# Kernel tuning notes

Hardware: AMD Instinct MI355X
Metric: run time of the kernel (lower is better)

## Reference

```python
import jax, jax.numpy as jnp
import numpy as np

B, S, D, H, HD, I, L = 1, 2048, 1024, 16, 64, 2816, 2
EPS = 1e-5
ROPE_BASE = 10000.0


def rmsnorm(x, w):
    return x * jax.lax.rsqrt(jnp.mean(x * x, axis=-1, keepdims=True) + EPS) * w


def precompute_freqs_cis():
    # matches precompute_freqs_cis: [S, HD//2, 2] = (cos, sin)
    freqs = 1.0 / (ROPE_BASE ** (jnp.arange(0, HD, 2, dtype=jnp.float32) / HD))
    ang = jnp.outer(jnp.arange(S, dtype=jnp.float32), freqs)
    return jnp.stack([jnp.cos(ang), jnp.sin(ang)], axis=-1)


def apply_rope(x, fc):
    # x: [B,S,H,HD]; fc: [S,HD//2,2] -> interleaved pair rotation
    xs = x.reshape(*x.shape[:-1], HD // 2, 2)
    f = fc[None, :, None]  # [1,S,1,HD//2,2]
    out = jnp.stack([
        xs[..., 0] * f[..., 0] - xs[..., 1] * f[..., 1],
        xs[..., 1] * f[..., 0] + xs[..., 0] * f[..., 1],
    ], axis=-1)
    return out.reshape(x.shape)


def setup_inputs() -> dict:
    key = jax.random.key(0)
    ks = jax.random.split(key, 6)
    p = lambda k, shape: jax.random.normal(k, shape, jnp.float32) * 0.02
    return {
        "x": jax.random.normal(ks[0], (B, S, D), jnp.float32),
        "wqkv": p(ks[1], (L, 3 * H * HD, D)),
        "wo": p(ks[2], (L, D, H * HD)),
        "w1": p(ks[3], (L, I, D)),
        "w2": p(ks[4], (L, D, I)),
        "w3": p(ks[5], (L, I, D)),
        "attn_norm_w": jnp.ones((L, D), jnp.float32),
        "ffn_norm_w": jnp.ones((L, D), jnp.float32),
        "attn_ls": 0.01 * jnp.ones((L, D), jnp.float32),
        "ffn_ls": 0.01 * jnp.ones((L, D), jnp.float32),
        "final_norm_w": jnp.ones((D,), jnp.float32),
    }


def reference(x, wqkv, wo, w1, w2, w3, attn_norm_w, ffn_norm_w, attn_ls, ffn_ls, final_norm_w):
    fc = precompute_freqs_cis()
    causal = jnp.tril(jnp.ones((S, S), dtype=bool))  # [S,S]
    scale = 1.0 / np.sqrt(HD).astype(np.float32)
    h = x
    for l in range(L):
        # --- attention block ---
        xn = rmsnorm(h, attn_norm_w[l])
        qkv = xn @ wqkv[l].T  # [B,S,3*H*HD]
        q, k, v = jnp.split(qkv, 3, axis=-1)
        q = apply_rope(q.reshape(B, S, H, HD), fc)
        k = apply_rope(k.reshape(B, S, H, HD), fc)
        v = v.reshape(B, S, H, HD)
        scores = jnp.einsum('bqhd,bkhd->bhqk', q, k) * scale
        scores = jnp.where(causal, scores, jnp.finfo(scores.dtype).min)
        attn = jax.nn.softmax(scores, axis=-1)
        y = jnp.einsum('bhqk,bkhd->bqhd', attn, v).reshape(B, S, H * HD)
        h = h + (y @ wo[l].T) * attn_ls[l]
        # --- feed-forward block (SwiGLU) ---
        xn = rmsnorm(h, ffn_norm_w[l])
        ff = (jax.nn.silu(xn @ w1[l].T) * (xn @ w3[l].T)) @ w2[l].T
        h = h + ff * ffn_ls[l]
    return rmsnorm(h, final_norm_w)
```

## Files before the change

kernel.cpp:

```cpp
#include <hip/hip_runtime.h>
#include <math.h>

#define SEQ 2048
#define DIM 1024
#define NH 16
#define HDIM 64
#define IDIM 2816
#define NL 2

typedef __attribute__((ext_vector_type(8))) short bf16x8;
typedef __attribute__((ext_vector_type(4))) float f32x4;

__device__ __forceinline__ unsigned short f2bf(float f) {
    unsigned int u = __float_as_uint(f);
    u = (u + 0x7fffu + ((u >> 16) & 1u)) >> 16;
    return (unsigned short)u;
}
__device__ __forceinline__ float bf2f(unsigned short u) {
    return __uint_as_float((unsigned int)u << 16);
}

__device__ __forceinline__ void gl_lds16(const void* g, void* l) {
    __builtin_amdgcn_global_load_lds(
        (const __attribute__((address_space(1))) unsigned int*)g,
        (__attribute__((address_space(3))) unsigned int*)l, 16, 0, 0);
}

template <bool BF16OUT>
__global__ __launch_bounds__(256) void rmsnorm_kernel(const float* __restrict__ in,
                                                      const float* __restrict__ w,
                                                      void* __restrict__ out) {
    const int row = blockIdx.x;
    const int t = threadIdx.x;
    const float4 v = ((const float4*)(in + (size_t)row * DIM))[t];
    float ss = v.x * v.x + v.y * v.y + v.z * v.z + v.w * v.w;
#pragma unroll
    for (int m = 1; m < 64; m <<= 1) ss += __shfl_xor(ss, m);
    __shared__ float red[4];
    if ((t & 63) == 0) red[t >> 6] = ss;
    __syncthreads();
    const float tot = red[0] + red[1] + red[2] + red[3];
    const float r = 1.0f / sqrtf(tot * (1.0f / DIM) + 1e-5f);
    const float4 wv = ((const float4*)w)[t];
    float o0 = v.x * r * wv.x, o1 = v.y * r * wv.y;
    float o2 = v.z * r * wv.z, o3 = v.w * r * wv.w;
    if (BF16OUT) {
        ushort4 o = {f2bf(o0), f2bf(o1), f2bf(o2), f2bf(o3)};
        ((ushort4*)((unsigned short*)out + (size_t)row * DIM))[t] = o;
    } else {
        float4 o = {o0, o1, o2, o3};
        ((float4*)((float*)out + (size_t)row * DIM))[t] = o;
    }
}

#define WQKV_OFF 0
#define WO_OFF   3145728
#define W1_OFF   4194304
#define W3_OFF   7077888
#define W2_OFF   9961472
#define WTOT     12845056

__global__ __launch_bounds__(256) void convert_weights_kernel(
    const float* __restrict__ wqkv, const float* __restrict__ wo,
    const float* __restrict__ w1, const float* __restrict__ w3,
    const float* __restrict__ w2, unsigned short* __restrict__ out) {
    const size_t i8 = ((size_t)blockIdx.x * 256 + threadIdx.x) * 8;
    const float* src;
    size_t local;
    if (i8 < WO_OFF)      { src = wqkv; local = i8 - WQKV_OFF; }
    else if (i8 < W1_OFF) { src = wo;   local = i8 - WO_OFF; }
    else if (i8 < W3_OFF) { src = w1;   local = i8 - W1_OFF; }
    else if (i8 < W2_OFF) { src = w3;   local = i8 - W3_OFF; }
    else                  { src = w2;   local = i8 - W2_OFF; }
    const float4 v0 = *(const float4*)(src + local);
    const float4 v1 = *(const float4*)(src + local + 4);
    ushort4 o0 = {f2bf(v0.x), f2bf(v0.y), f2bf(v0.z), f2bf(v0.w)};
    ushort4 o1 = {f2bf(v1.x), f2bf(v1.y), f2bf(v1.z), f2bf(v1.w)};
    *(ushort4*)(out + i8) = o0;
    *(ushort4*)(out + i8 + 4) = o1;
}

template <int EPI, int BM, int BN>
__global__ __launch_bounds__(256) void mfma_gemm(
    const unsigned short* __restrict__ A,
    const unsigned short* __restrict__ B,
    const unsigned short* __restrict__ Bhi, int nsplit,
    float* __restrict__ Cf,
    unsigned short* __restrict__ Cb,
    const float* __restrict__ ls,
    int N, int K) {
    constexpr int MI = BM / 32;
    constexpr int NJ = BN / 32;
    __shared__ unsigned short As[2][BM * 32];
    __shared__ unsigned short Bs[2][BN * 32];

    const int tid = threadIdx.x;

    const int nwg = gridDim.x * gridDim.y;
    const int orig = blockIdx.y * gridDim.x + blockIdx.x;
    const int swz = (orig & 7) * (nwg >> 3) + (orig >> 3);
    const int bx = swz % gridDim.x;
    const int by = swz / gridDim.x;
    const int m0 = by * BM;
    const int ncol0 = bx * BN;

    const unsigned short* Bp = B;
    int n0 = ncol0;
    if (n0 >= nsplit) { Bp = Bhi; n0 -= nsplit; }

    const int srow = tid >> 2;
    const int skof = (tid & 3) * 8;
    const unsigned short* Ag = A + (size_t)(m0 + srow) * K + skof;
    const unsigned short* Bg = Bp + (size_t)(n0 + srow) * K + skof;

    const int lane = tid & 63;
    const int wid = tid >> 6;
    const int wr = (wid >> 1) * (BM / 2);
    const int wc = (wid & 1) * (BN / 2);
    const int fr = lane & 15;
    const int fk = (lane >> 4) * 8;

    f32x4 acc[MI][NJ] = {};

#define STAGE(buf, kk)                                                        \
    {                                                                         \
        _Pragma("unroll")                                                     \
        for (int p = 0; p < BM / 64; ++p)                                     \
            gl_lds16(Ag + (size_t)(p * 64) * K + (kk),                        \
                     &As[buf][p * 2048 + tid * 8]);                           \
        _Pragma("unroll")                                                     \
        for (int p = 0; p < BN / 64; ++p)                                     \
            gl_lds16(Bg + (size_t)(p * 64) * K + (kk),                        \
                     &Bs[buf][p * 2048 + tid * 8]);                           \
    }

    STAGE(0, 0);
    __syncthreads();
    int cur = 0;
    for (int k0 = 0; k0 < K; k0 += 32) {
        if (k0 + 32 < K) STAGE(cur ^ 1, k0 + 32);
        bf16x8 a[MI], b[NJ];
#pragma unroll
        for (int m = 0; m < MI; ++m)
            a[m] = *(const bf16x8*)&As[cur][(wr + m * 16 + fr) * 32 + fk];
#pragma unroll
        for (int n = 0; n < NJ; ++n)
            b[n] = *(const bf16x8*)&Bs[cur][(wc + n * 16 + fr) * 32 + fk];
        __builtin_amdgcn_s_setprio(1);
#pragma unroll
        for (int m = 0; m < MI; ++m)
#pragma unroll
            for (int n = 0; n < NJ; ++n)
                acc[m][n] = __builtin_amdgcn_mfma_f32_16x16x32_bf16(a[m], b[n], acc[m][n], 0, 0, 0);
        __builtin_amdgcn_s_setprio(0);
        __syncthreads();
        cur ^= 1;
    }
#undef STAGE

    const int erow = m0 + wr + (lane >> 4) * 4;
    const int ecol = ncol0 + wc + fr;
#pragma unroll
    for (int m = 0; m < MI; ++m) {
#pragma unroll
        for (int n = 0; n < NJ; ++n) {
            const f32x4 v = acc[m][n];
            const int row = erow + m * 16;
            const int col = ecol + n * 16;
            if (EPI == 1) {
                const float lv = ls[col];
#pragma unroll
                for (int j = 0; j < 4; ++j) {
                    float* p = Cf + (size_t)(row + j) * N + col;
                    *p = *p + v[j] * lv;
                }
            } else {
#pragma unroll
                for (int j = 0; j < 4; ++j)
                    Cb[(size_t)(row + j) * N + col] = f2bf(v[j]);
            }
        }
    }
}

__global__ __launch_bounds__(256) void silu_mul_kernel(
    const unsigned short* __restrict__ c13,
    unsigned short* __restrict__ outp) {
    const size_t e8 = ((size_t)blockIdx.x * 256 + threadIdx.x) * 8;
    const int m = (int)(e8 / IDIM);
    const int i = (int)(e8 % IDIM);
    const unsigned short* g = c13 + (size_t)m * (2 * IDIM) + i;
    const bf16x8 gv = *(const bf16x8*)g;
    const bf16x8 uv = *(const bf16x8*)(g + IDIM);
    unsigned short o[8];
#pragma unroll
    for (int j = 0; j < 8; ++j) {
        const float x = bf2f((unsigned short)gv[j]);
        const float u = bf2f((unsigned short)uv[j]);
        o[j] = f2bf(x / (1.0f + __expf(-x)) * u);
    }
    *(bf16x8*)(outp + (size_t)m * IDIM + i) = *(const bf16x8*)o;
}

__global__ __launch_bounds__(256) void rope_split_kernel(
    const unsigned short* __restrict__ qkv,
    unsigned short* __restrict__ Qh,
    unsigned short* __restrict__ Kh,
    unsigned short* __restrict__ Vt) {
    const int st = blockIdx.x;
    const int h = blockIdx.y;
    const int tid = threadIdx.x;
    const int srow = tid >> 2;
    const int scol = (tid & 3) * 16;
    const int s = st * 64 + srow;
    __shared__ unsigned short Vl[64][72];

    const unsigned short* base = qkv + (size_t)s * (3 * DIM) + h * HDIM + scol;

    unsigned short qv[16], kv[16], vv[16];
    *(bf16x8*)&qv[0] = *(const bf16x8*)(base);
    *(bf16x8*)&qv[8] = *(const bf16x8*)(base + 8);
    *(bf16x8*)&kv[0] = *(const bf16x8*)(base + DIM);
    *(bf16x8*)&kv[8] = *(const bf16x8*)(base + DIM + 8);
    *(bf16x8*)&vv[0] = *(const bf16x8*)(base + 2 * DIM);
    *(bf16x8*)&vv[8] = *(const bf16x8*)(base + 2 * DIM + 8);

    unsigned short qo[16], ko[16];
#pragma unroll
    for (int i = 0; i < 8; ++i) {
        const int p = scol / 2 + i;
        const float freq = powf(10000.0f, -(float)(2 * p) * (1.0f / 64.0f));
        const float ang = (float)s * freq;
        float sn, cs;
        sincosf(ang, &sn, &cs);
        const float q0 = bf2f(qv[2 * i]), q1 = bf2f(qv[2 * i + 1]);
        const float k0 = bf2f(kv[2 * i]), k1 = bf2f(kv[2 * i + 1]);
        qo[2 * i]     = f2bf(q0 * cs - q1 * sn);
        qo[2 * i + 1] = f2bf(q1 * cs + q0 * sn);
        ko[2 * i]     = f2bf(k0 * cs - k1 * sn);
        ko[2 * i + 1] = f2bf(k1 * cs + k0 * sn);
    }
    unsigned short* qdst = Qh + ((size_t)h * SEQ + s) * HDIM + scol;
    unsigned short* kdst = Kh + ((size_t)h * SEQ + s) * HDIM + scol;
    *(bf16x8*)qdst = *(const bf16x8*)&qo[0];
    *(bf16x8*)(qdst + 8) = *(const bf16x8*)&qo[8];
    *(bf16x8*)kdst = *(const bf16x8*)&ko[0];
    *(bf16x8*)(kdst + 8) = *(const bf16x8*)&ko[8];

#pragma unroll
    for (int i = 0; i < 16; ++i) Vl[scol + i][srow] = vv[i];
    __syncthreads();
    const int d = tid >> 2;
    const int c0 = (tid & 3) * 16;
    unsigned short* vdst = Vt + ((size_t)h * HDIM + d) * SEQ + st * 64 + c0;
    *(bf16x8*)vdst = *(const bf16x8*)&Vl[d][c0];
    *(bf16x8*)(vdst + 8) = *(const bf16x8*)&Vl[d][c0 + 8];
}

__global__ __launch_bounds__(256) void attn_mfma_kernel(
    const unsigned short* __restrict__ Qh,
    const unsigned short* __restrict__ Kh,
    const unsigned short* __restrict__ Vt,
    unsigned short* __restrict__ y) {
    const int h = blockIdx.x;
    const int qt = blockIdx.y;
    const int qb = (qt < 16) ? qt : 47 - qt;

    __shared__ unsigned short Ql[64][72];
    __shared__ unsigned short Kl[2][64][72];
    __shared__ unsigned short Vl[2][64][72];
    __shared__ unsigned short Pl[64][72];

    const int tid = threadIdx.x;
    const int lane = tid & 63;
    const int w = tid >> 6;
    const int fr = lane & 15;
    const int fk = (lane >> 4) * 8;
    const int rg = (lane >> 4) * 4;
    const int srow = tid >> 2;
    const int sc8 = (tid & 3) * 8;

    {
        const unsigned short* src = Qh + ((size_t)h * SEQ + qb * 64 + srow) * HDIM + sc8;
        *(bf16x8*)&Ql[srow][sc8] = *(const bf16x8*)src;
        *(bf16x8*)&Ql[srow][sc8 + 32] = *(const bf16x8*)(src + 32);
    }
    __syncthreads();
    bf16x8 qa[2];
    qa[0] = *(const bf16x8*)&Ql[w * 16 + fr][fk];
    qa[1] = *(const bf16x8*)&Ql[w * 16 + fr][32 + fk];

    bf16x8 kr0, kr1, vr0, vr1;
    {
        const unsigned short* ks = Kh + ((size_t)h * SEQ + srow) * HDIM + sc8;
        kr0 = *(const bf16x8*)ks;
        kr1 = *(const bf16x8*)(ks + 32);
        const unsigned short* vs = Vt + ((size_t)h * HDIM + srow) * SEQ + sc8;
        vr0 = *(const bf16x8*)vs;
        vr1 = *(const bf16x8*)(vs + 32);
    }

    float l_[4] = {0.0f, 0.0f, 0.0f, 0.0f};
    f32x4 O[4] = {};

    for (int kb = 0; kb <= qb; ++kb) {
        const int cur = kb & 1;
        *(bf16x8*)&Kl[cur][srow][sc8] = kr0;
        *(bf16x8*)&Kl[cur][srow][sc8 + 32] = kr1;
        *(bf16x8*)&Vl[cur][srow][sc8] = vr0;
        *(bf16x8*)&Vl[cur][srow][sc8 + 32] = vr1;
        __syncthreads();

        if (kb < qb) {
            const unsigned short* ks = Kh + ((size_t)h * SEQ + (kb + 1) * 64 + srow) * HDIM + sc8;
            kr0 = *(const bf16x8*)ks;
            kr1 = *(const bf16x8*)(ks + 32);
            const unsigned short* vs = Vt + ((size_t)h * HDIM + srow) * SEQ + (kb + 1) * 64 + sc8;
            vr0 = *(const bf16x8*)vs;
            vr1 = *(const bf16x8*)(vs + 32);
        }

        f32x4 sa[4] = {};
        __builtin_amdgcn_s_setprio(1);
#pragma unroll
        for (int ks2 = 0; ks2 < 2; ++ks2)
#pragma unroll
            for (int n = 0; n < 4; ++n) {
                const bf16x8 kf = *(const bf16x8*)&Kl[cur][n * 16 + fr][ks2 * 32 + fk];
                sa[n] = __builtin_amdgcn_mfma_f32_16x16x32_bf16(qa[ks2], kf, sa[n], 0, 0, 0);
            }
        __builtin_amdgcn_s_setprio(0);

        const bool diag = (kb == qb);
#pragma unroll
        for (int n = 0; n < 4; ++n) {
            const int col = n * 16 + fr;
#pragma unroll
            for (int j = 0; j < 4; ++j) {
                const float sv = sa[n][j] * 0.125f;
                float e = __expf(fminf(sv, 30.0f));
                if (diag && col > rg + j) e = 0.0f;
                l_[j] += e;
                Pl[w * 16 + rg + j][col] = f2bf(e);
            }
        }

        __builtin_amdgcn_s_setprio(1);
#pragma unroll
        for (int ks2 = 0; ks2 < 2; ++ks2) {
            const bf16x8 pa = *(const bf16x8*)&Pl[w * 16 + fr][ks2 * 32 + fk];
#pragma unroll
            for (int nd = 0; nd < 4; ++nd) {
                const bf16x8 vf = *(const bf16x8*)&Vl[cur][nd * 16 + fr][ks2 * 32 + fk];
                O[nd] = __builtin_amdgcn_mfma_f32_16x16x32_bf16(pa, vf, O[nd], 0, 0, 0);
            }
        }
        __builtin_amdgcn_s_setprio(0);
    }

#pragma unroll
    for (int j = 0; j < 4; ++j) {
#pragma unroll
        for (int msk = 1; msk < 16; msk <<= 1) l_[j] += __shfl_xor(l_[j], msk);
    }

#pragma unroll
    for (int j = 0; j < 4; ++j) {
        const float inv = 1.0f / l_[j];
        unsigned short* dst = y + (size_t)(qb * 64 + w * 16 + rg + j) * DIM + h * HDIM + fr;
#pragma unroll
        for (int nd = 0; nd < 4; ++nd)
            dst[nd * 16] = f2bf(O[nd][j] * inv);
    }
}

extern "C" void kernel_launch(void* const* d_in, const int* in_sizes, int n_in,
                              void* d_out, int out_size, void* d_ws, size_t ws_size,
                              hipStream_t stream) {
    const float* x            = (const float*)d_in[0];
    const float* wqkv         = (const float*)d_in[1];
    const float* wo           = (const float*)d_in[2];
    const float* w1           = (const float*)d_in[3];
    const float* w2           = (const float*)d_in[4];
    const float* w3           = (const float*)d_in[5];
    const float* attn_norm_w  = (const float*)d_in[6];
    const float* ffn_norm_w   = (const float*)d_in[7];
    const float* attn_ls      = (const float*)d_in[8];
    const float* ffn_ls       = (const float*)d_in[9];
    const float* final_norm_w = (const float*)d_in[10];
    float* out = (float*)d_out;

    char* ws = (char*)d_ws;
    float*          h     = (float*)ws;
    unsigned short* xnb   = (unsigned short*)(ws + 8388608);
    unsigned short* yb    = (unsigned short*)(ws + 12582912);
    unsigned short* qkvb  = (unsigned short*)(ws + 16777216);
    unsigned short* Qhb   = (unsigned short*)(ws + 29360128);
    unsigned short* Khb   = (unsigned short*)(ws + 33554432);
    unsigned short* Vtb   = (unsigned short*)(ws + 37748736);
    unsigned short* c13   = (unsigned short*)(ws + 16777216);
    unsigned short* ffb   = (unsigned short*)(ws + 41943040);
    unsigned short* wbuf  = (unsigned short*)(ws + 46137344);

    unsigned short* wqkv_b = wbuf + WQKV_OFF;
    unsigned short* wo_b   = wbuf + WO_OFF;
    unsigned short* w1_b   = wbuf + W1_OFF;
    unsigned short* w3_b   = wbuf + W3_OFF;
    unsigned short* w2_b   = wbuf + W2_OFF;

    const int BIG = 1 << 30;

    hipMemcpyAsync(h, x, (size_t)SEQ * DIM * sizeof(float),
                   hipMemcpyDeviceToDevice, stream);

    for (int l = 0; l < NL; ++l) {
        convert_weights_kernel<<<WTOT / 2048, 256, 0, stream>>>(
            wqkv + (size_t)l * 3 * DIM * DIM, wo + (size_t)l * DIM * DIM,
            w1 + (size_t)l * IDIM * DIM, w3 + (size_t)l * IDIM * DIM,
            w2 + (size_t)l * DIM * IDIM, wbuf);

        rmsnorm_kernel<true><<<SEQ, 256, 0, stream>>>(h, attn_norm_w + l * DIM, xnb);
        mfma_gemm<3, 128, 128><<<dim3(3 * DIM / 128, SEQ / 128), 256, 0, stream>>>(
            xnb, wqkv_b, nullptr, BIG, nullptr, qkvb, nullptr, 3 * DIM, DIM);
        rope_split_kernel<<<dim3(SEQ / 64, NH), 256, 0, stream>>>(qkvb, Qhb, Khb, Vtb);
        attn_mfma_kernel<<<dim3(NH, SEQ / 64), 256, 0, stream>>>(Qhb, Khb, Vtb, yb);
        mfma_gemm<1, 64, 128><<<dim3(DIM / 128, SEQ / 64), 256, 0, stream>>>(
            yb, wo_b, nullptr, BIG, h, nullptr, attn_ls + l * DIM, DIM, DIM);

        rmsnorm_kernel<true><<<SEQ, 256, 0, stream>>>(h, ffn_norm_w + l * DIM, xnb);
        mfma_gemm<3, 128, 128><<<dim3(2 * IDIM / 128, SEQ / 128), 256, 0, stream>>>(
            xnb, w1_b, w3_b, IDIM, nullptr, c13, nullptr, 2 * IDIM, DIM);
        silu_mul_kernel<<<SEQ * IDIM / 2048, 256, 0, stream>>>(c13, ffb);
        mfma_gemm<1, 64, 128><<<dim3(DIM / 128, SEQ / 64), 256, 0, stream>>>(
            ffb, w2_b, nullptr, BIG, h, nullptr, ffn_ls + l * DIM, DIM, IDIM);
    }

    rmsnorm_kernel<false><<<SEQ, 256, 0, stream>>>(h, final_norm_w, out);
}
```

Measured before the change: 413.8 us.

## Deepen GEMM global-to-LDS pipeline to four stages with explicit vmcnt waits

Moves the MFMA GEMM from double buffering to a four-stage LDS ring. Global-to-LDS loads for tiles up to three steps ahead stay in flight, and manual s_waitcnt vmcnt counts plus pinned barriers replace the per-iteration __syncthreads. The aim is to hide global memory latency behind more MFMA work. In exchange LDS use doubles, which may reduce occupancy, and correctness now depends on the hand-computed vmcnt values matching the number of loads per stage.

```diff
diff --git a/kernel.cpp b/kernel.cpp
--- a/kernel.cpp
+++ b/kernel.cpp
@@ -25,6 +25,13 @@
         (const __attribute__((address_space(1))) unsigned int*)g,
         (__attribute__((address_space(3))) unsigned int*)l, 16, 0, 0);
 }
+
+#define WAITVM(n) asm volatile("s_waitcnt vmcnt(" #n ")" ::: "memory")
+#define BARRIER_PIN()                       \
+    do {                                    \
+        __builtin_amdgcn_s_barrier();       \
+        __builtin_amdgcn_sched_barrier(0);  \
+    } while (0)
 
 template <bool BF16OUT>
 __global__ __launch_bounds__(256) void rmsnorm_kernel(const float* __restrict__ in,
@@ -91,8 +98,9 @@
     int N, int K) {
     constexpr int MI = BM / 32;
     constexpr int NJ = BN / 32;
-    __shared__ unsigned short As[2][BM * 32];
-    __shared__ unsigned short Bs[2][BN * 32];
+    constexpr int L = BM / 64 + BN / 64;
+    __shared__ unsigned short As[4][BM * 32];
+    __shared__ unsigned short Bs[4][BN * 32];
 
     const int tid = threadIdx.x;
 
@@ -134,18 +142,14 @@
                      &Bs[buf][p * 2048 + tid * 8]);                           \
     }
 
-    STAGE(0, 0);
-    __syncthreads();
-    int cur = 0;
-    for (int k0 = 0; k0 < K; k0 += 32) {
-        if (k0 + 32 < K) STAGE(cur ^ 1, k0 + 32);
+    auto compute_tile = [&](int buf) {
         bf16x8 a[MI], b[NJ];
 #pragma unroll
         for (int m = 0; m < MI; ++m)
-            a[m] = *(const bf16x8*)&As[cur][(wr + m * 16 + fr) * 32 + fk];
+            a[m] = *(const bf16x8*)&As[buf][(wr + m * 16 + fr) * 32 + fk];
 #pragma unroll
         for (int n = 0; n < NJ; ++n)
-            b[n] = *(const bf16x8*)&Bs[cur][(wc + n * 16 + fr) * 32 + fk];
+            b[n] = *(const bf16x8*)&Bs[buf][(wc + n * 16 + fr) * 32 + fk];
         __builtin_amdgcn_s_setprio(1);
 #pragma unroll
         for (int m = 0; m < MI; ++m)
@@ -153,9 +157,36 @@
             for (int n = 0; n < NJ; ++n)
                 acc[m][n] = __builtin_amdgcn_mfma_f32_16x16x32_bf16(a[m], b[n], acc[m][n], 0, 0, 0);
         __builtin_amdgcn_s_setprio(0);
-        __syncthreads();
-        cur ^= 1;
-    }
+    };
+
+    const int NT = K / 32;
+
+    STAGE(0, 0);
+    STAGE(1, 32);
+    STAGE(2, 64);
+    STAGE(3, 96);
+
+    for (int t = 0; t < NT - 3; ++t) {
+        if constexpr (L == 3) WAITVM(9); else WAITVM(12);
+        BARRIER_PIN();
+        compute_tile(t & 3);
+        asm volatile("s_waitcnt lgkmcnt(0)" ::: "memory");
+        BARRIER_PIN();
+        if (t + 4 < NT) STAGE(t & 3, (t + 4) * 32);
+    }
+    if constexpr (L == 3) WAITVM(6); else WAITVM(8);
+    BARRIER_PIN();
+    compute_tile((NT - 3) & 3);
+    asm volatile("s_waitcnt lgkmcnt(0)" ::: "memory");
+    BARRIER_PIN();
+    if constexpr (L == 3) WAITVM(3); else WAITVM(4);
+    BARRIER_PIN();
+    compute_tile((NT - 2) & 3);
+    asm volatile("s_waitcnt lgkmcnt(0)" ::: "memory");
+    BARRIER_PIN();
+    WAITVM(0);
+    BARRIER_PIN();
+    compute_tile((NT - 1) & 3);
 #undef STAGE
 
     const int erow = m0 + wr + (lane >> 4) * 4;
```

Result: slower. 424.5 us (+2.6%).
